# Kernel tuning notes

Hardware: AMD Instinct MI355X
Metric: run time of the kernel (lower is better)

The kernel has to match this reference:

```python
import jax, jax.numpy as jnp
import numpy as np

N, E, F_IN, HID, HEADS, OUT_DIM, G = 50000, 600000, 92, 32, 8, 1, 512
EPS = 1e-5


def setup_inputs() -> dict:
    key = jax.random.key(0)
    ks = jax.random.split(key, 30)
    s = 0.1
    d1 = HID * HEADS  # 256
    inp = {
        "x": jax.random.normal(ks[0], (N, F_IN), dtype=jnp.float32),
        "edge_index": jax.random.randint(ks[1], (2, E), 0, N),
        "edge_attr": jax.random.uniform(ks[2], (E, 1), dtype=jnp.float32),
        "batch": jnp.sort(jax.random.randint(ks[3], (N,), 0, G)),
        # conv1 (heads=8, concat)
        "W1": jax.random.normal(ks[4], (F_IN, d1)) * s,
        "We1": jax.random.normal(ks[5], (1, d1)) * s,
        "as1": jax.random.normal(ks[6], (HEADS, HID)) * s,
        "ad1": jax.random.normal(ks[7], (HEADS, HID)) * s,
        "ae1": jax.random.normal(ks[8], (HEADS, HID)) * s,
        "b1": jax.random.normal(ks[9], (d1,)) * s,
        # bn1 (eval mode, running stats)
        "g1": jnp.ones((d1,)), "be1": jnp.zeros((d1,)),
        "m1": jax.random.normal(ks[10], (d1,)) * s, "v1": jnp.ones((d1,)),
        # conv2 (heads=1)
        "W2": jax.random.normal(ks[11], (d1, HID)) * s,
        "We2": jax.random.normal(ks[12], (1, HID)) * s,
        "as2": jax.random.normal(ks[13], (1, HID)) * s,
        "ad2": jax.random.normal(ks[14], (1, HID)) * s,
        "ae2": jax.random.normal(ks[15], (1, HID)) * s,
        "b2": jax.random.normal(ks[16], (HID,)) * s,
        # bn2
        "g2": jnp.ones((HID,)), "be2": jnp.zeros((HID,)),
        "m2": jax.random.normal(ks[17], (HID,)) * s, "v2": jnp.ones((HID,)),
        # final fc
        "fcW": jax.random.normal(ks[18], (HID, OUT_DIM)) * s,
        "fcb": jnp.zeros((OUT_DIM,)),
    }
    return inp


def _gat_conv(x, edge_index, edge_attr, W, We, a_s, a_d, a_e, b, heads, ch):
    """PyG GATConv with edge_dim, add_self_loops=True (fill_value='mean'), concat."""
    n = x.shape[0]
    src, dst = edge_index[0], edge_index[1]
    # self loops: loop edge_attr = mean of incoming edge_attr per node
    cnt = jax.ops.segment_sum(jnp.ones((edge_attr.shape[0],), edge_attr.dtype), dst, n)
    loop_attr = jax.ops.segment_sum(edge_attr, dst, n) / jnp.clip(cnt, 1.0)[:, None]
    ar = jnp.arange(n)
    src = jnp.concatenate([src, ar])
    dst = jnp.concatenate([dst, ar])
    ea = jnp.concatenate([edge_attr, loop_attr], axis=0)
    h = (x @ W).reshape(n, heads, ch)                 # [N,H,C]
    al_s = jnp.sum(h * a_s, axis=-1)                  # [N,H]
    al_d = jnp.sum(h * a_d, axis=-1)                  # [N,H]
    he = (ea @ We).reshape(-1, heads, ch)             # [E',H,C]
    al_e = jnp.sum(he * a_e, axis=-1)                 # [E',H]
    alpha = jax.nn.leaky_relu(al_s[src] + al_d[dst] + al_e, 0.2)
    # scatter softmax over destination segments
    mx = jax.ops.segment_max(alpha, dst, n)
    w = jnp.exp(alpha - mx[dst])
    den = jax.ops.segment_sum(w, dst, n)
    w = w / den[dst]                                  # [E',H]
    out = jax.ops.segment_sum(h[src] * w[:, :, None], dst, n)  # [N,H,C]
    return out.reshape(n, heads * ch) + b


def _bn_eval(x, g, b, m, v):
    return (x - m) * (g / jnp.sqrt(v + EPS)) + b


def reference(x, edge_index, edge_attr, batch,
              W1, We1, as1, ad1, ae1, b1, g1, be1, m1, v1,
              W2, We2, as2, ad2, ae2, b2, g2, be2, m2, v2,
              fcW, fcb):
    h = _gat_conv(x, edge_index, edge_attr, W1, We1, as1, ad1, ae1, b1, HEADS, HID)
    h = jax.nn.relu(_bn_eval(h, g1, be1, m1, v1))
    # dropout is identity in eval mode
    h = _gat_conv(h, edge_index, edge_attr, W2, We2, as2, ad2, ae2, b2, 1, HID)
    h = jax.nn.relu(_bn_eval(h, g2, be2, m2, v2))
    # global mean pool over graphs
    sums = jax.ops.segment_sum(h, batch, G)
    cnt = jax.ops.segment_sum(jnp.ones((h.shape[0],), h.dtype), batch, G)
    pooled = sums / jnp.clip(cnt, 1.0)[:, None]
    return pooled @ fcW + fcb
```

## Files before the change

kernel.cpp:

```cpp
#include <hip/hip_runtime.h>
#include <hip/hip_bf16.h>

#define N_NODES 50000
#define N_EDGES 600000
#define F_IN    92
#define KPAD    96
#define HID     32
#define HEADS   8
#define D1      256
#define G_GRAPHS 512
#define EPSV    1e-5f
#define NCHUNK  49
#define DEGBLK  2344
#define FILLBLK 2344

using short8  = __attribute__((ext_vector_type(8))) short;
using f32x4   = __attribute__((ext_vector_type(4))) float;
using f32x2   = __attribute__((ext_vector_type(2))) float;

__device__ __forceinline__ float bf2f(unsigned short u) {
    return __uint_as_float(((unsigned)u) << 16);
}
__device__ __forceinline__ unsigned short f2bf(float f) {
    unsigned u = __float_as_uint(f);
    return (unsigned short)((u + 0x7FFFu + ((u >> 16) & 1u)) >> 16);
}


__global__ __launch_bounds__(256) void k_deg_setup(
        const int* __restrict__ ei, int* __restrict__ deg,
        const float* __restrict__ W1, const float* __restrict__ W2,
        const float* __restrict__ We1, const float* __restrict__ ae1,
        const float* __restrict__ We2, const float* __restrict__ ae2,
        const float* __restrict__ as1, const float* __restrict__ ad1,
        const float* __restrict__ b1, const float* __restrict__ g1,
        const float* __restrict__ be1, const float* __restrict__ m1,
        const float* __restrict__ v1,
        const float* __restrict__ b2, const float* __restrict__ g2,
        const float* __restrict__ be2, const float* __restrict__ m2,
        const float* __restrict__ v2,
        unsigned short* __restrict__ W1p, unsigned short* __restrict__ W2p,
        float* __restrict__ va, float* __restrict__ wedot,
        float* __restrict__ bnA1, float* __restrict__ bnB1,
        float* __restrict__ bnA2, float* __restrict__ bnB2) {
    int blk = blockIdx.x, t = threadIdx.x;
    if (blk < DEGBLK) {
        int e = blk * 256 + t;
        if (e < N_EDGES) atomicAdd(&deg[ei[N_EDGES + e]], 1);
        return;
    }
    int b = blk - DEGBLK;
    if (b < 96) {
        int gid = b * 256 + t;
        int k = gid >> 8, col = gid & 255;
        unsigned short v = 0;
        if (k < F_IN) v = f2bf(W1[k * D1 + col]);
        W1p[(((k >> 3) * D1) + col) * 8 + (k & 7)] = v;
    } else if (b < 128) {
        int gid = (b - 96) * 256 + t;
        int k = gid >> 5, col = gid & 31;
        W2p[(((k >> 3) * 32) + col) * 8 + (k & 7)] = f2bf(W2[gid]);
    } else if (b < 134) {
        int gid = (b - 128) * 256 + t;
        if (gid < 2 * HEADS * F_IN) {
            int which = gid / (HEADS * F_IN), rem = gid % (HEADS * F_IN);
            int h = rem / F_IN, k = rem % F_IN;
            const float* av = which ? ad1 : as1;
            float s = 0.f;
            #pragma unroll 8
            for (int c = 0; c < HID; ++c) s += W1[k * D1 + h * HID + c] * av[h * HID + c];
            va[gid] = s;
        }
    } else if (b == 134) {
        if (t < HEADS) {
            float a = 0.f;
            for (int c = 0; c < HID; ++c) a += We1[t * HID + c] * ae1[t * HID + c];
            wedot[t] = a;
        } else if (t == HEADS) {
            float a = 0.f;
            for (int c = 0; c < HID; ++c) a += We2[c] * ae2[c];
            wedot[HEADS] = a;
        }
    } else {
        if (t < D1) {
            float sc = g1[t] * __frsqrt_rn(v1[t] + EPSV);
            bnA1[t] = sc;
            bnB1[t] = (b1[t] - m1[t]) * sc + be1[t];
        }
        if (t < HID) {
            float sc = g2[t] * __frsqrt_rn(v2[t] + EPSV);
            bnA2[t] = sc;
            bnB2[t] = (b2[t] - m2[t]) * sc + be2[t];
        }
    }
}

__global__ void k_partial(const int* __restrict__ deg, int* __restrict__ partials) {
    int b = blockIdx.x;
    int s = 0;
    for (int j = 0; j < 4; ++j) {
        int i = b * 1024 + j * 256 + threadIdx.x;
        if (i < N_NODES) s += deg[i];
    }
    for (int off = 32; off; off >>= 1) s += __shfl_down(s, off, 64);
    __shared__ int sm[4];
    if ((threadIdx.x & 63) == 0) sm[threadIdx.x >> 6] = s;
    __syncthreads();
    if (threadIdx.x == 0) partials[b] = sm[0] + sm[1] + sm[2] + sm[3];
}

__global__ void k_scanc(const int* __restrict__ deg, const int* __restrict__ partials,
                        int* __restrict__ row_off, int* __restrict__ cursor) {
    int b = blockIdx.x;
    int t = threadIdx.x;
    __shared__ int smp;
    if (t < 64) {
        int pv = (t < b) ? partials[t] : 0;
        #pragma unroll
        for (int off = 32; off; off >>= 1) pv += __shfl_down(pv, off, 64);
        if (t == 0) smp = pv;
    }
    int base_i = b * 1024 + t * 4;
    int v[4]; int s = 0;
    #pragma unroll
    for (int j = 0; j < 4; ++j) {
        int i = base_i + j;
        v[j] = (i < N_NODES) ? deg[i] : 0;
        s += v[j];
    }
    __shared__ int sm[256];
    sm[t] = s;
    __syncthreads();
    int val = s;
    for (int off = 1; off < 256; off <<= 1) {
        int add = (t >= off) ? sm[t - off] : 0;
        __syncthreads();
        val += add;
        sm[t] = val;
        __syncthreads();
    }
    int base = smp + (val - s);
    #pragma unroll
    for (int j = 0; j < 4; ++j) {
        int i = base_i + j;
        if (i < N_NODES) { row_off[i] = base; cursor[i] = base; }
        base += v[j];
    }
}

__global__ __launch_bounds__(256) void k_fill_conv1(
        const int* __restrict__ ei, const float* __restrict__ ea,
        int* __restrict__ cursor, int2* __restrict__ adj,
        const float* __restrict__ x,
        const unsigned short* __restrict__ W1p,
        const float* __restrict__ va,
        unsigned char* __restrict__ h1f8,
        float* __restrict__ al_s,
        float* __restrict__ al_d) {
    __shared__ float xs[16 * F_IN];
    __shared__ unsigned short xbs[16 * KPAD];
    __shared__ float hs[16 * D1];
    int t = threadIdx.x;
    if (blockIdx.x < FILLBLK) {
        int e = blockIdx.x * 256 + t;
        if (e < N_EDGES) {
            int d = ei[N_EDGES + e];
            int pos = atomicAdd(&cursor[d], 1);
            adj[pos] = make_int2(ei[e], __float_as_int(ea[e]));
        }
        return;
    }
    int n0 = (blockIdx.x - FILLBLK) * 16;
    for (int i = t; i < 16 * F_IN; i += 256)
        xs[i] = x[(size_t)n0 * F_IN + i];
    __syncthreads();
    for (int i = t; i < 16 * KPAD; i += 256) {
        int r = i / KPAD, k = i - r * KPAD;
        xbs[i] = (k < F_IN) ? f2bf(xs[r * F_IN + k]) : (unsigned short)0;
    }
    {
        int r = t >> 4, j = t & 15;
        const float* vp = va + j * F_IN;
        const float* xr = xs + r * F_IN;
        float s = 0.f;
        for (int k = 0; k < F_IN; ++k) s += xr[k] * vp[k];
        if (j < 8) al_s[(n0 + r) * HEADS + j] = s;
        else       al_d[(n0 + r) * HEADS + (j - 8)] = s;
    }
    __syncthreads();
    int wid = t >> 6, l = t & 63;
    int g = l >> 4, c16 = l & 15;
    const short8* xb = (const short8*)(xbs + c16 * KPAD + g * 8);
    short8 af0 = xb[0], af1 = xb[4], af2 = xb[8];
    const short8* wp = (const short8*)W1p;
    #pragma unroll
    for (int ct = 0; ct < 4; ++ct) {
        int col = (wid * 4 + ct) * 16 + c16;
        f32x4 acc = {0.f, 0.f, 0.f, 0.f};
        acc = __builtin_amdgcn_mfma_f32_16x16x32_bf16(af0, wp[(0 * 4 + g) * D1 + col], acc, 0, 0, 0);
        acc = __builtin_amdgcn_mfma_f32_16x16x32_bf16(af1, wp[(1 * 4 + g) * D1 + col], acc, 0, 0, 0);
        acc = __builtin_amdgcn_mfma_f32_16x16x32_bf16(af2, wp[(2 * 4 + g) * D1 + col], acc, 0, 0, 0);
        #pragma unroll
        for (int r = 0; r < 4; ++r)
            hs[(g * 4 + r) * D1 + col] = acc[r];
    }
    __syncthreads();
    {
        int r = t >> 4, grp = t & 15;
        const float* src = hs + r * D1 + grp * 16;
        int d[4];
        #pragma unroll
        for (int j = 0; j < 4; ++j) {
            int lo = __builtin_amdgcn_cvt_pk_fp8_f32(src[j * 4 + 0], src[j * 4 + 1], 0, false);
            d[j]   = __builtin_amdgcn_cvt_pk_fp8_f32(src[j * 4 + 2], src[j * 4 + 3], lo, true);
        }
        *(int4*)(h1f8 + (size_t)(n0 + r) * D1 + grp * 16) = make_int4(d[0], d[1], d[2], d[3]);
    }
}

__global__ __launch_bounds__(256) void k_aggr1(
        const int* __restrict__ row_off, const int* __restrict__ deg,
        const int2* __restrict__ adj,
        const unsigned char* __restrict__ h1f8,
        const float* __restrict__ al_s, const float* __restrict__ al_d,
        const float* __restrict__ wedot,
        const float* __restrict__ bnA1, const float* __restrict__ bnB1,
        unsigned short* __restrict__ h1p) {
    int wid = threadIdx.x >> 6, l = threadIdx.x & 63;
    int n = blockIdx.x * 4 + wid;
    if (n >= N_NODES) return;
    int h = l >> 3;
    float wd = wedot[h];
    float dn = al_d[n * HEADS + h];
    int r0 = row_off[n], cnt = deg[n];
    float a0 = 0.f, a1 = 0.f, a2 = 0.f, a3 = 0.f, den = 0.f, ea_sum = 0.f;
    for (int base = 0; base < cnt; base += 64) {
        int m = cnt - base; if (m > 64) m = 64;
        int sl = 0; float el = 0.f;
        if (l < m) {
            int2 se = adj[r0 + base + l];
            sl = se.x;
            el = __int_as_float(se.y);
        }
        for (int i = 0; i < m; ++i) {
            int s = __shfl(sl, i, 64);
            float eav = __shfl(el, i, 64);
            float a = al_s[s * HEADS + h] + dn + eav * wd;
            a = a > 0.f ? a : 0.2f * a;
            float w = __expf(a);
            den += w;
            ea_sum += eav;
            unsigned w8 = *(const unsigned*)(h1f8 + (size_t)s * D1 + l * 4);
            f32x2 lo = __builtin_amdgcn_cvt_pk_f32_fp8(w8, false);
            f32x2 hi = __builtin_amdgcn_cvt_pk_f32_fp8(w8, true);
            a0 += w * lo.x; a1 += w * lo.y;
            a2 += w * hi.x; a3 += w * hi.y;
        }
    }
    {
        float la = ea_sum / (float)(cnt > 0 ? cnt : 1);
        float a = al_s[n * HEADS + h] + dn + la * wd;
        a = a > 0.f ? a : 0.2f * a;
        float w = __expf(a);
        den += w;
        unsigned w8 = *(const unsigned*)(h1f8 + (size_t)n * D1 + l * 4);
        f32x2 lo = __builtin_amdgcn_cvt_pk_f32_fp8(w8, false);
        f32x2 hi = __builtin_amdgcn_cvt_pk_f32_fp8(w8, true);
        a0 += w * lo.x; a1 += w * lo.y;
        a2 += w * hi.x; a3 += w * hi.y;
    }
    float inv = 1.f / den;
    int c = l * 4;
    float4 A = *(const float4*)(bnA1 + c);
    float4 B = *(const float4*)(bnB1 + c);
    ushort4 o;
    o.x = f2bf(fmaxf(a0 * inv * A.x + B.x, 0.f));
    o.y = f2bf(fmaxf(a1 * inv * A.y + B.y, 0.f));
    o.z = f2bf(fmaxf(a2 * inv * A.z + B.z, 0.f));
    o.w = f2bf(fmaxf(a3 * inv * A.w + B.w, 0.f));
    *(ushort4*)(h1p + (size_t)n * D1 + c) = o;
}


__global__ __launch_bounds__(256) void k_gemm2(const unsigned short* __restrict__ h1p,
                                               const unsigned short* __restrict__ W2p,
                                               const float* __restrict__ as2,
                                               const float* __restrict__ ad2,
                                               unsigned char* __restrict__ h2f8,
                                               float* __restrict__ al_s2,
                                               float* __restrict__ al_d2) {
    int wid = threadIdx.x >> 6, l = threadIdx.x & 63;
    int wave = blockIdx.x * 4 + wid;
    if (wave >= N_NODES / 16) return;
    int n0 = wave * 16;
    int g = l >> 4;
    int c16 = l & 15;
    f32x4 acc0 = {0.f, 0.f, 0.f, 0.f};
    f32x4 acc1 = {0.f, 0.f, 0.f, 0.f};
    const short8* ap = (const short8*)(h1p + (size_t)(n0 + c16) * D1 + g * 8);
    const short8* wp = (const short8*)W2p;
    #pragma unroll
    for (int ks = 0; ks < 8; ++ks) {
        short8 afrag = ap[ks * 4];
        short8 b0 = wp[(ks * 4 + g) * 32 + c16];
        short8 b1 = wp[(ks * 4 + g) * 32 + 16 + c16];
        acc0 = __builtin_amdgcn_mfma_f32_16x16x32_bf16(afrag, b0, acc0, 0, 0, 0);
        acc1 = __builtin_amdgcn_mfma_f32_16x16x32_bf16(afrag, b1, acc1, 0, 0, 0);
    }
    float s0 = as2[c16], s1 = as2[16 + c16];
    float d0 = ad2[c16], d1 = ad2[16 + c16];
    float ps[4], pd[4];
    #pragma unroll
    for (int r = 0; r < 4; ++r) {
        int node = n0 + g * 4 + r;
        int p0 = __builtin_amdgcn_cvt_pk_fp8_f32(acc0[r], acc0[r], 0, false);
        int p1 = __builtin_amdgcn_cvt_pk_fp8_f32(acc1[r], acc1[r], 0, false);
        h2f8[(size_t)node * HID + c16]      = (unsigned char)p0;
        h2f8[(size_t)node * HID + 16 + c16] = (unsigned char)p1;
        ps[r] = acc0[r] * s0 + acc1[r] * s1;
        pd[r] = acc0[r] * d0 + acc1[r] * d1;
    }
    #pragma unroll
    for (int off = 1; off < 16; off <<= 1) {
        #pragma unroll
        for (int r = 0; r < 4; ++r) {
            ps[r] += __shfl_xor(ps[r], off, 64);
            pd[r] += __shfl_xor(pd[r], off, 64);
        }
    }
    if (c16 == 0) {
        #pragma unroll
        for (int r = 0; r < 4; ++r) {
            int node = n0 + g * 4 + r;
            al_s2[node] = ps[r];
            al_d2[node] = pd[r];
        }
    }
}

__global__ __launch_bounds__(256) void k_aggr2(
        const int* __restrict__ row_off, const int* __restrict__ deg,
        const int2* __restrict__ adj,
        const unsigned char* __restrict__ h2f8,
        const float* __restrict__ al_s2, const float* __restrict__ al_d2,
        const float* __restrict__ wedot,
        const float* __restrict__ bnA2, const float* __restrict__ bnB2,
        float* __restrict__ h2p) {
    int wid = threadIdx.x >> 6, l = threadIdx.x & 63;
    int n = blockIdx.x * 4 + wid;
    if (n >= N_NODES) return;
    int g = l >> 3, c8 = l & 7;
    float wd = wedot[HEADS];
    float dn = al_d2[n];
    int r0 = row_off[n], cnt = deg[n];
    float a0 = 0.f, a1 = 0.f, a2 = 0.f, a3 = 0.f, den = 0.f, ea_sum = 0.f;
    for (int base = 0; base < cnt; base += 64) {
        int m = cnt - base; if (m > 64) m = 64;
        int sl = 0; float el = 0.f;
        if (l < m) {
            int2 se = adj[r0 + base + l];
            sl = se.x;
            el = __int_as_float(se.y);
        }
        for (int i = 0; i < m; i += 8) {
            int j = i + g;
            int jj = j < m ? j : 0;
            int s = __shfl(sl, jj, 64);
            float eav = __shfl(el, jj, 64);
            if (j < m) {
                float a = al_s2[s] + dn + eav * wd;
                a = a > 0.f ? a : 0.2f * a;
                float w = __expf(a);
                den += w;
                ea_sum += eav;
                unsigned w8 = *(const unsigned*)(h2f8 + (size_t)s * HID + c8 * 4);
                f32x2 lo = __builtin_amdgcn_cvt_pk_f32_fp8(w8, false);
                f32x2 hi = __builtin_amdgcn_cvt_pk_f32_fp8(w8, true);
                a0 += w * lo.x; a1 += w * lo.y;
                a2 += w * hi.x; a3 += w * hi.y;
            }
        }
    }
    #pragma unroll
    for (int off = 8; off < 64; off <<= 1) {
        a0 += __shfl_xor(a0, off, 64);
        a1 += __shfl_xor(a1, off, 64);
        a2 += __shfl_xor(a2, off, 64);
        a3 += __shfl_xor(a3, off, 64);
        den += __shfl_xor(den, off, 64);
        ea_sum += __shfl_xor(ea_sum, off, 64);
    }
    {
        float la = ea_sum / (float)(cnt > 0 ? cnt : 1);
        float a = al_s2[n] + dn + la * wd;
        a = a > 0.f ? a : 0.2f * a;
        float w = __expf(a);
        den += w;
        unsigned w8 = *(const unsigned*)(h2f8 + (size_t)n * HID + c8 * 4);
        f32x2 lo = __builtin_amdgcn_cvt_pk_f32_fp8(w8, false);
        f32x2 hi = __builtin_amdgcn_cvt_pk_f32_fp8(w8, true);
        a0 += w * lo.x; a1 += w * lo.y;
        a2 += w * hi.x; a3 += w * hi.y;
    }
    if (g == 0) {
        float inv = 1.f / den;
        int c = c8 * 4;
        float4 A = *(const float4*)(bnA2 + c);
        float4 B = *(const float4*)(bnB2 + c);
        float4 y;
        y.x = fmaxf(a0 * inv * A.x + B.x, 0.f);
        y.y = fmaxf(a1 * inv * A.y + B.y, 0.f);
        y.z = fmaxf(a2 * inv * A.z + B.z, 0.f);
        y.w = fmaxf(a3 * inv * A.w + B.w, 0.f);
        *(float4*)(h2p + (size_t)n * HID + c) = y;
    }
}

__global__ __launch_bounds__(64) void k_poolfc(const float* __restrict__ h2p,
                                               const int* __restrict__ batch,
                                               const float* __restrict__ fcW,
                                               const float* __restrict__ fcb,
                                               float* __restrict__ out) {
    int g = blockIdx.x;
    int l = threadIdx.x;
    auto lb = [&](int key) {
        int lo = 0, hi = N_NODES;
        while (lo < hi) {
            int mid = (lo + hi) >> 1;
            if (batch[mid] < key) lo = mid + 1; else hi = mid;
        }
        return lo;
    };
    int s0 = lb(g), s1 = lb(g + 1);
    int c = l & 31, half = l >> 5;
    float acc = 0.f;
    for (int r = s0 + half; r < s1; r += 2)
        acc += h2p[(size_t)r * HID + c];
    acc += __shfl_xor(acc, 32, 64);
    int cn = s1 - s0;
    float mean = acc / (float)(cn > 0 ? cn : 1);
    float p = mean * fcW[c];
    #pragma unroll
    for (int off = 1; off < 32; off <<= 1) p += __shfl_xor(p, off, 64);
    if (l == 0) out[g] = p + fcb[0];
}


extern "C" void kernel_launch(void* const* d_in, const int* in_sizes, int n_in,
                              void* d_out, int out_size, void* d_ws, size_t ws_size,
                              hipStream_t stream) {
    const float* x    = (const float*)d_in[0];
    const int*   ei   = (const int*)  d_in[1];
    const float* ea   = (const float*)d_in[2];
    const int*   batch= (const int*)  d_in[3];
    const float* W1   = (const float*)d_in[4];
    const float* We1  = (const float*)d_in[5];
    const float* as1  = (const float*)d_in[6];
    const float* ad1  = (const float*)d_in[7];
    const float* ae1  = (const float*)d_in[8];
    const float* b1   = (const float*)d_in[9];
    const float* g1   = (const float*)d_in[10];
    const float* be1  = (const float*)d_in[11];
    const float* m1   = (const float*)d_in[12];
    const float* v1   = (const float*)d_in[13];
    const float* W2   = (const float*)d_in[14];
    const float* We2  = (const float*)d_in[15];
    const float* as2  = (const float*)d_in[16];
    const float* ad2  = (const float*)d_in[17];
    const float* ae2  = (const float*)d_in[18];
    const float* b2   = (const float*)d_in[19];
    const float* g2   = (const float*)d_in[20];
    const float* be2  = (const float*)d_in[21];
    const float* m2   = (const float*)d_in[22];
    const float* v2   = (const float*)d_in[23];
    const float* fcW  = (const float*)d_in[24];
    const float* fcb  = (const float*)d_in[25];
    float* out = (float*)d_out;

    char* ws = (char*)d_ws;
    size_t off = 0;
    auto alloc = [&](size_t bytes) -> void* {
        void* p = ws + off;
        off += (bytes + 255) & ~(size_t)255;
        return p;
    };
    int*   deg     = (int*)  alloc((size_t)N_NODES * 4);
    int*   row_off = (int*)  alloc((size_t)N_NODES * 4);
    int*   cursor  = (int*)  alloc((size_t)N_NODES * 4);
    int2*  adj     = (int2*) alloc((size_t)N_EDGES * 8);
    float* al_s1   = (float*)alloc((size_t)N_NODES * HEADS * 4);
    float* al_d1   = (float*)alloc((size_t)N_NODES * HEADS * 4);
    float* al_s2   = (float*)alloc((size_t)N_NODES * 4);
    float* al_d2   = (float*)alloc((size_t)N_NODES * 4);
    float* wedot   = (float*)alloc(16 * 4);
    float* va      = (float*)alloc((size_t)2 * HEADS * F_IN * 4);
    int*   partials= (int*)  alloc(64 * 4);
    float* bnA1    = (float*)alloc((size_t)D1 * 4);
    float* bnB1    = (float*)alloc((size_t)D1 * 4);
    float* bnA2    = (float*)alloc((size_t)HID * 4);
    float* bnB2    = (float*)alloc((size_t)HID * 4);
    unsigned short* W1p = (unsigned short*)alloc((size_t)KPAD * D1 * 2);
    unsigned short* W2p = (unsigned short*)alloc((size_t)D1 * HID * 2);
    unsigned char*  h1f8 = (unsigned char*)alloc((size_t)N_NODES * D1);
    unsigned short* h1p = (unsigned short*)alloc((size_t)N_NODES * D1 * 2);
    unsigned char*  h2f8 = (unsigned char*)alloc((size_t)N_NODES * HID);
    float* h2p     = (float*)alloc((size_t)N_NODES * HID * 4);
    (void)ws_size; (void)in_sizes; (void)n_in; (void)out_size;

    hipMemsetAsync(deg, 0, (size_t)N_NODES * 4, stream);

    k_deg_setup<<<DEGBLK + 136, 256, 0, stream>>>(ei, deg, W1, W2, We1, ae1, We2, ae2,
                                                  as1, ad1, b1, g1, be1, m1, v1,
                                                  b2, g2, be2, m2, v2,
                                                  W1p, W2p, va, wedot,
                                                  bnA1, bnB1, bnA2, bnB2);
    k_partial<<<NCHUNK, 256, 0, stream>>>(deg, partials);
    k_scanc<<<NCHUNK, 256, 0, stream>>>(deg, partials, row_off, cursor);
    k_fill_conv1<<<FILLBLK + N_NODES / 16, 256, 0, stream>>>(ei, ea, cursor, adj,
                                                             x, W1p, va, h1f8,
                                                             al_s1, al_d1);
    k_aggr1<<<(N_NODES + 3) / 4, 256, 0, stream>>>(row_off, deg, adj,
                                                   h1f8, al_s1, al_d1, wedot,
                                                   bnA1, bnB1, h1p);

    k_gemm2<<<(N_NODES / 16 + 3) / 4, 256, 0, stream>>>(h1p, W2p, as2, ad2, h2f8, al_s2, al_d2);
    k_aggr2<<<(N_NODES + 3) / 4, 256, 0, stream>>>(row_off, deg, adj,
                                                   h2f8, al_s2, al_d2, wedot, bnA2, bnB2, h2p);
    k_poolfc<<<G_GRAPHS, 64, 0, stream>>>(h2p, batch, fcW, fcb, out);
}
```

Baseline: 214.1 us.

## Split fill and conv1 kernels, pad shared tile, conflict-free fp8 packing

Splits the fused edge-fill/conv1 kernel into two separate launches, so the fill blocks no longer carry conv1's large shared-memory footprint and the two parts can be occupancy-tuned independently. The hs shared tile gets a padded leading dimension (264) to reduce LDS bank conflicts on the MFMA result stores. The fp8 packing step now reads strided 4-element groups and writes 4-byte stores instead of one 16-byte store per thread, which spreads LDS reads across banks. The cost is an extra kernel launch and the loss of overlap between the atomic fill work and the GEMM work.

```diff
diff --git a/kernel.cpp b/kernel.cpp
--- a/kernel.cpp
+++ b/kernel.cpp
@@ -8,11 +8,11 @@
 #define HID     32
 #define HEADS   8
 #define D1      256
+#define HS_LD   264
 #define G_GRAPHS 512
 #define EPSV    1e-5f
 #define NCHUNK  49
 #define DEGBLK  2344
-#define FILLBLK 2344
 
 using short8  = __attribute__((ext_vector_type(8))) short;
 using f32x4   = __attribute__((ext_vector_type(4))) float;
@@ -148,29 +148,27 @@
     }
 }
 
-__global__ __launch_bounds__(256) void k_fill_conv1(
-        const int* __restrict__ ei, const float* __restrict__ ea,
-        int* __restrict__ cursor, int2* __restrict__ adj,
-        const float* __restrict__ x,
-        const unsigned short* __restrict__ W1p,
-        const float* __restrict__ va,
-        unsigned char* __restrict__ h1f8,
-        float* __restrict__ al_s,
-        float* __restrict__ al_d) {
+__global__ void k_fill(const int* __restrict__ ei, const float* __restrict__ ea,
+                       int* __restrict__ cursor, int2* __restrict__ adj) {
+    int e = blockIdx.x * 256 + threadIdx.x;
+    if (e < N_EDGES) {
+        int d = ei[N_EDGES + e];
+        int pos = atomicAdd(&cursor[d], 1);
+        adj[pos] = make_int2(ei[e], __float_as_int(ea[e]));
+    }
+}
+
+__global__ __launch_bounds__(256) void k_conv1(const float* __restrict__ x,
+                                               const unsigned short* __restrict__ W1p,
+                                               const float* __restrict__ va,
+                                               unsigned char* __restrict__ h1f8,
+                                               float* __restrict__ al_s,
+                                               float* __restrict__ al_d) {
     __shared__ float xs[16 * F_IN];
     __shared__ unsigned short xbs[16 * KPAD];
-    __shared__ float hs[16 * D1];
+    __shared__ float hs[16 * HS_LD];
+    int n0 = blockIdx.x * 16;
     int t = threadIdx.x;
-    if (blockIdx.x < FILLBLK) {
-        int e = blockIdx.x * 256 + t;
-        if (e < N_EDGES) {
-            int d = ei[N_EDGES + e];
-            int pos = atomicAdd(&cursor[d], 1);
-            adj[pos] = make_int2(ei[e], __float_as_int(ea[e]));
-        }
-        return;
-    }
-    int n0 = (blockIdx.x - FILLBLK) * 16;
     for (int i = t; i < 16 * F_IN; i += 256)
         xs[i] = x[(size_t)n0 * F_IN + i];
     __syncthreads();
@@ -202,19 +200,18 @@
         acc = __builtin_amdgcn_mfma_f32_16x16x32_bf16(af2, wp[(2 * 4 + g) * D1 + col], acc, 0, 0, 0);
         #pragma unroll
         for (int r = 0; r < 4; ++r)
-            hs[(g * 4 + r) * D1 + col] = acc[r];
+            hs[(g * 4 + r) * HS_LD + col] = acc[r];
     }
     __syncthreads();
     {
-        int r = t >> 4, grp = t & 15;
-        const float* src = hs + r * D1 + grp * 16;
-        int d[4];
+        int r = t >> 4, q = t & 15;
         #pragma unroll
         for (int j = 0; j < 4; ++j) {
-            int lo = __builtin_amdgcn_cvt_pk_fp8_f32(src[j * 4 + 0], src[j * 4 + 1], 0, false);
-            d[j]   = __builtin_amdgcn_cvt_pk_fp8_f32(src[j * 4 + 2], src[j * 4 + 3], lo, true);
-        }
-        *(int4*)(h1f8 + (size_t)(n0 + r) * D1 + grp * 16) = make_int4(d[0], d[1], d[2], d[3]);
+            const float* src = hs + r * HS_LD + q * 4 + j * 64;
+            int lo = __builtin_amdgcn_cvt_pk_fp8_f32(src[0], src[1], 0, false);
+            int pk = __builtin_amdgcn_cvt_pk_fp8_f32(src[2], src[3], lo, true);
+            *(int*)(h1f8 + (size_t)(n0 + r) * D1 + q * 4 + j * 64) = pk;
+        }
     }
 }
 
@@ -516,9 +513,9 @@
                                                   bnA1, bnB1, bnA2, bnB2);
     k_partial<<<NCHUNK, 256, 0, stream>>>(deg, partials);
     k_scanc<<<NCHUNK, 256, 0, stream>>>(deg, partials, row_off, cursor);
-    k_fill_conv1<<<FILLBLK + N_NODES / 16, 256, 0, stream>>>(ei, ea, cursor, adj,
-                                                             x, W1p, va, h1f8,
-                                                             al_s1, al_d1);
+    k_fill<<<(N_EDGES + 255) / 256, 256, 0, stream>>>(ei, ea, cursor, adj);
+
+    k_conv1<<<N_NODES / 16, 256, 0, stream>>>(x, W1p, va, h1f8, al_s1, al_d1);
     k_aggr1<<<(N_NODES + 3) / 4, 256, 0, stream>>>(row_off, deg, adj,
                                                    h1f8, al_s1, al_d1, wedot,
                                                    bnA1, bnB1, h1p);
```

After: 214.3 us. Within noise of the previous version (+0.1%).
